# Optimization experiments

Measured on AMD Instinct MI355X. Metric: run time of the kernel, lower is better.

## Reference

```python
import jax, jax.numpy as jnp
import numpy as np

NUM_HEADS = 8
KEY_DIM = 16
D_V = 32  # attn_ratio * key_dim


def _conv1x1_bn(x, w, s, b):
    # x: [B, Cin, H, W], w: [Cout, Cin]; 1x1 conv == channel contraction,
    # eval-mode BatchNorm folded into per-channel scale s and bias b.
    y = jnp.einsum('bchw,oc->bohw', x, w)
    return y * s[:, None, None] + b[:, None, None]


def setup_inputs() -> dict:
    key = jax.random.key(0)
    ks = jax.random.split(key, 14)
    B, C, H, W = 16, 256, 32, 32
    nh_kd, dh = NUM_HEADS * KEY_DIM, NUM_HEADS * D_V
    f = jax.random.normal
    return {
        'x': f(ks[0], (B, C, H, W), jnp.float32),
        'wq': f(ks[1], (nh_kd, C), jnp.float32) * 0.05,
        'sq': jax.random.uniform(ks[2], (nh_kd,), jnp.float32),
        'bq': f(ks[3], (nh_kd,), jnp.float32) * 0.05,
        'wk': f(ks[4], (nh_kd, C), jnp.float32) * 0.05,
        'sk': jax.random.uniform(ks[5], (nh_kd,), jnp.float32),
        'bk': f(ks[6], (nh_kd,), jnp.float32) * 0.05,
        'wv': f(ks[7], (dh, C), jnp.float32) * 0.05,
        'sv': jax.random.uniform(ks[8], (dh,), jnp.float32),
        'bv': f(ks[9], (dh,), jnp.float32) * 0.05,
        'wp': f(ks[10], (C, dh), jnp.float32) * 0.05,
        'sp': jax.random.uniform(ks[11], (C,), jnp.float32),
        'bp': f(ks[12], (C,), jnp.float32) * 0.05,
    }


def reference(x, wq, sq, bq, wk, sk, bk, wv, sv, bv, wp, sp, bp):
    B, C, H, W = x.shape
    N = H * W
    # QKV projections (1x1 conv + folded BN)
    q = _conv1x1_bn(x, wq, sq, bq).reshape(B, NUM_HEADS, KEY_DIM, N)  # b h k n
    k = _conv1x1_bn(x, wk, sk, bk).reshape(B, NUM_HEADS, KEY_DIM, N)  # b h k m
    v = _conv1x1_bn(x, wv, sv, bv).reshape(B, NUM_HEADS, D_V, N)      # b h d m
    # NOTE: the original forward does NOT apply self.scale to the scores.
    attn = jnp.einsum('bhkn,bhkm->bhnm', q, k)
    attn = jax.nn.softmax(attn, axis=-1)
    out = jnp.einsum('bhnm,bhdm->bhdn', attn, v)  # b h d n
    out = out.reshape(B, NUM_HEADS * D_V, H, W)
    # proj = Sequential(activation, Conv2d_BN): activation FIRST
    out = jax.nn.relu(out)
    return _conv1x1_bn(out, wp, sp, bp)
```

## Files before the change

kernel.cpp:

```cpp
#include <hip/hip_runtime.h>

#define NTOT 1024
#define CIN  256
#define BATCH 16
#define NH   8
#define KD   16
#define DV   32
#define L2E  1.44269504088896340736f

typedef unsigned short u16;
typedef unsigned int   u32;
typedef __attribute__((ext_vector_type(8)))  _Float16 f16x8;
typedef __attribute__((ext_vector_type(16))) float    f32x16;

__device__ inline f16x8 as_f16x8(uint4 u) { return __builtin_bit_cast(f16x8, u); }
__device__ inline u32 pkrtz(float a, float b) {
  return __builtin_bit_cast(u32, __builtin_amdgcn_cvt_pkrtz(a, b));
}
__device__ inline u16 f2h(float x) {
  return __builtin_bit_cast(u16, (_Float16)x);
}
__device__ inline float fexp2(float x) {
#if __has_builtin(__builtin_amdgcn_exp2f)
  return __builtin_amdgcn_exp2f(x);
#else
  float r; asm("v_exp_f32 %0, %1" : "=v"(r) : "v"(x)); return r;
#endif
}

__global__ __launch_bounds__(64) void prep_weights(
    const float* __restrict__ wq, const float* __restrict__ sq, const float* __restrict__ bq,
    const float* __restrict__ wk, const float* __restrict__ sk, const float* __restrict__ bk,
    const float* __restrict__ wv, const float* __restrict__ sv, const float* __restrict__ bv,
    const float* __restrict__ wp, const float* __restrict__ sp, const float* __restrict__ bp,
    u16* __restrict__ wqkv, u16* __restrict__ wph, float* __restrict__ ball)
{
  const int row = blockIdx.x;
  const int t = threadIdx.x;
  const float* src; u16* dst; float sc, bi;
  if (row < 128)      { src = wq + (size_t)row*CIN;       sc = sq[row]*L2E;     bi = bq[row]*L2E;     dst = wqkv + (size_t)row*CIN; }
  else if (row < 256) { src = wk + (size_t)(row-128)*CIN; sc = sk[row-128];     bi = bk[row-128];     dst = wqkv + (size_t)row*CIN; }
  else if (row < 512) { src = wv + (size_t)(row-256)*CIN; sc = sv[row-256];     bi = bv[row-256];     dst = wqkv + (size_t)row*CIN; }
  else                { src = wp + (size_t)(row-512)*CIN; sc = sp[row-512];     bi = bp[row-512];     dst = wph + (size_t)(row-512)*CIN; }
  const float4 v = *(const float4*)&src[t*4];
  ushort4 r;
  r.x = f2h(v.x*sc); r.y = f2h(v.y*sc); r.z = f2h(v.z*sc); r.w = f2h(v.w*sc);
  *(ushort4*)&dst[t*4] = r;
  if (t == 0) ball[row] = bi;
}

__global__ __launch_bounds__(256) void transpose_x(
    const float* __restrict__ X, u16* __restrict__ Xt)
{
  __shared__ u16 T[64][64];
  const int t  = threadIdx.x;
  const int n0 = blockIdx.x * 64;
  const int c0 = blockIdx.y * 64;
  const int b  = blockIdx.z;
  #pragma unroll
  for (int rr = 0; rr < 4; ++rr) {
    const int c  = rr*16 + (t>>4);
    const int n4 = (t&15)*4;
    const float4 v = *(const float4*)&X[((size_t)b*CIN + c0 + c)*NTOT + n0 + n4];
    ushort4 r; r.x=f2h(v.x); r.y=f2h(v.y); r.z=f2h(v.z); r.w=f2h(v.w);
    *(ushort4*)&T[c][n4] = r;
  }
  __syncthreads();
  const int nl = t & 63;
  #pragma unroll
  for (int j = 0; j < 2; ++j) {
    const int oct = (t>>6)*2 + j;
    uint4 w;
    w.x = (u32)T[oct*8+0][nl] | ((u32)T[oct*8+1][nl] << 16);
    w.y = (u32)T[oct*8+2][nl] | ((u32)T[oct*8+3][nl] << 16);
    w.z = (u32)T[oct*8+4][nl] | ((u32)T[oct*8+5][nl] << 16);
    w.w = (u32)T[oct*8+6][nl] | ((u32)T[oct*8+7][nl] << 16);
    *(uint4*)&Xt[((size_t)b*NTOT + n0 + nl)*CIN + c0 + oct*8] = w;
  }
}

template<int BN, int MODE>
__global__ __launch_bounds__(256) void conv_mfma(
    const u16* __restrict__ Wh, const u16* __restrict__ Bt,
    const float* __restrict__ ball,
    u16* __restrict__ q_t, u16* __restrict__ k_t, u16* __restrict__ v_h,
    float* __restrict__ outp)
{
  constexpr int FN = BN / 64;
  __shared__ u16 A_lds[128 * 64];
  __shared__ u16 B_lds[BN * 64];
  const int t    = threadIdx.x;
  const int lane = t & 63;
  const int w    = t >> 6;
  const int wm = w >> 1, wn = w & 1;
  const int g = lane >> 5, nl = lane & 31;
  const int n0 = blockIdx.x * BN;
  const int m0 = blockIdx.y * 128;
  const int b  = blockIdx.z;

  f32x16 acc[2][FN] = {};

  for (int c0 = 0; c0 < CIN; c0 += 64) {
    #pragma unroll
    for (int r = 0; r < 4; ++r) {
      const int idx = t + r*256;
      const int row = idx >> 3, ch = idx & 7;
      const uint4 v = *(const uint4*)&Wh[(size_t)(m0+row)*CIN + c0 + ch*8];
      *(uint4*)&A_lds[row*64 + ((ch ^ (row&7))*8)] = v;
    }
    #pragma unroll
    for (int r = 0; r < BN/32; ++r) {
      const int idx = t + r*256;
      const int row = idx >> 3, ch = idx & 7;
      const uint4 v = *(const uint4*)&Bt[((size_t)b*NTOT + n0 + row)*CIN + c0 + ch*8];
      *(uint4*)&B_lds[row*64 + ((ch ^ (row&7))*8)] = v;
    }
    __syncthreads();
    #pragma unroll
    for (int ks = 0; ks < 4; ++ks) {
      const int ch = 2*ks + g;
      f16x8 a[2], bb[FN];
      #pragma unroll
      for (int fi = 0; fi < 2; ++fi) {
        const int row = wm*64 + fi*32 + nl;
        a[fi] = as_f16x8(*(const uint4*)&A_lds[row*64 + ((ch ^ (row&7))*8)]);
      }
      #pragma unroll
      for (int fj = 0; fj < FN; ++fj) {
        const int row = wn*(BN/2) + fj*32 + nl;
        bb[fj] = as_f16x8(*(const uint4*)&B_lds[row*64 + ((ch ^ (row&7))*8)]);
      }
      #pragma unroll
      for (int fi = 0; fi < 2; ++fi)
        #pragma unroll
        for (int fj = 0; fj < FN; ++fj)
          acc[fi][fj] = __builtin_amdgcn_mfma_f32_32x32x16_f16(a[fi], bb[fj], acc[fi][fj], 0, 0, 0);
    }
    __syncthreads();
  }

  #pragma unroll
  for (int fi = 0; fi < 2; ++fi) {
    #pragma unroll
    for (int fj = 0; fj < FN; ++fj) {
      const int n = n0 + wn*(BN/2) + fj*32 + nl;
      #pragma unroll
      for (int q = 0; q < 4; ++q) {
        const int ob = m0 + wm*64 + fi*32 + 8*q + 4*g;
        const float v0 = acc[fi][fj][4*q+0] + ball[ob+0];
        const float v1 = acc[fi][fj][4*q+1] + ball[ob+1];
        const float v2 = acc[fi][fj][4*q+2] + ball[ob+2];
        const float v3 = acc[fi][fj][4*q+3] + ball[ob+3];
        if (MODE == 0) {
          if (ob < 128) {
            const int h = ob >> 4, k0 = ob & 15;
            ushort4 r; r.x = f2h(v0); r.y = f2h(v1); r.z = f2h(v2); r.w = f2h(v3);
            *(ushort4*)&q_t[(((size_t)b*NH + h)*NTOT + n)*KD + k0] = r;
          } else if (ob < 256) {
            const int oo = ob - 128;
            const int h = oo >> 4, k0 = oo & 15;
            const int plane = k0 >> 3, j0 = k0 & 7;
            ushort4 r; r.x = f2h(v0); r.y = f2h(v1); r.z = f2h(v2); r.w = f2h(v3);
            *(ushort4*)&k_t[((((size_t)b*NH + h)*2 + plane)*NTOT + n)*8 + j0] = r;
          } else {
            const int oo = ob - 256;
            const int h = oo >> 5, d0 = oo & 31;
            const int mb = n >> 4, loc = n & 15;
            const int g2 = (loc >> 2) & 1;
            const int j  = (loc & 3) + ((loc >> 3) << 2);
            u16* vp = v_h + (((((size_t)b*NH + h)*64 + mb)*2 + g2)*32 + d0)*8 + j;
            vp[0*8] = f2h(v0);
            vp[1*8] = f2h(v1);
            vp[2*8] = f2h(v2);
            vp[3*8] = f2h(v3);
          }
        } else {
          float* op = outp + ((size_t)b*CIN + ob)*NTOT + n;
          op[0*NTOT] = v0; op[1*NTOT] = v1; op[2*NTOT] = v2; op[3*NTOT] = v3;
        }
      }
    }
  }
}

__global__ __launch_bounds__(1024) void attn_mfma(
    const u16* __restrict__ Qt,
    const u16* __restrict__ Kt,
    const u16* __restrict__ Vt,
    u16* __restrict__ Ot)
{
  __shared__ u16 K_lds[2*NTOT*8];
  __shared__ u16 V_lds[4096*8];
  const int t    = threadIdx.x;
  const int lane = t & 63;
  const int wave = t >> 6;
  const int bh   = blockIdx.x >> 1;
  const int half = blockIdx.x & 1;
  const int g = lane >> 5, nl = lane & 31;
  const int n0 = half*512 + wave*32;

  const u16* Kh = Kt + (size_t)bh*(2*NTOT*8);
  const u16* Vh = Vt + (size_t)bh*(4096*8);
  const u16* Qh = Qt + (size_t)bh*(NTOT*KD);

  #pragma unroll
  for (int r = 0; r < 2; ++r) {
    const int uu = r*1024 + t;
    *(uint4*)&K_lds[uu*8] = *(const uint4*)&Kh[uu*8];
  }
  #pragma unroll
  for (int r = 0; r < 4; ++r) {
    const int uu = r*1024 + t;
    *(uint4*)&V_lds[uu*8] = *(const uint4*)&Vh[uu*8];
  }

  const f16x8 qf = as_f16x8(*(const uint4*)&Qh[(size_t)(n0+nl)*KD + g*8]);
  __syncthreads();

  const f32x16 fzero = {};
  f32x16 acc = {};
  float l = 0.f;
  const char* Kb = (const char*)K_lds + g*16384 + nl*16;
  const char* Vb = (const char*)V_lds + g*512   + nl*16;

  f16x8 kf  = as_f16x8(*(const uint4*)(Kb));
  uint4 va0 = *(const uint4*)(Vb);
  uint4 va1 = *(const uint4*)(Vb + 1024);

  #pragma unroll 4
  for (int st = 0; st < 31; ++st) {
    const f32x16 s = __builtin_amdgcn_mfma_f32_32x32x16_f16(kf, qf, fzero, 0, 0, 0);
    kf  = as_f16x8(*(const uint4*)(Kb + (st+1)*512));
    const uint4 nva0 = *(const uint4*)(Vb + (st+1)*2048);
    const uint4 nva1 = *(const uint4*)(Vb + (st+1)*2048 + 1024);

    float p[16];
    #pragma unroll
    for (int r = 0; r < 16; ++r) p[r] = fexp2(s[r]);
    l += (((p[0]+p[1])+(p[2]+p[3])) + ((p[4]+p[5])+(p[6]+p[7])))
       + (((p[8]+p[9])+(p[10]+p[11])) + ((p[12]+p[13])+(p[14]+p[15])));

    uint4 b0, b1;
    b0.x = pkrtz(p[0],  p[1]);  b0.y = pkrtz(p[2],  p[3]);
    b0.z = pkrtz(p[4],  p[5]);  b0.w = pkrtz(p[6],  p[7]);
    b1.x = pkrtz(p[8],  p[9]);  b1.y = pkrtz(p[10], p[11]);
    b1.z = pkrtz(p[12], p[13]); b1.w = pkrtz(p[14], p[15]);

    acc = __builtin_amdgcn_mfma_f32_32x32x16_f16(as_f16x8(va0), as_f16x8(b0), acc, 0, 0, 0);
    acc = __builtin_amdgcn_mfma_f32_32x32x16_f16(as_f16x8(va1), as_f16x8(b1), acc, 0, 0, 0);
    va0 = nva0; va1 = nva1;
  }
  {
    const f32x16 s = __builtin_amdgcn_mfma_f32_32x32x16_f16(kf, qf, fzero, 0, 0, 0);
    float p[16];
    #pragma unroll
    for (int r = 0; r < 16; ++r) p[r] = fexp2(s[r]);
    l += (((p[0]+p[1])+(p[2]+p[3])) + ((p[4]+p[5])+(p[6]+p[7])))
       + (((p[8]+p[9])+(p[10]+p[11])) + ((p[12]+p[13])+(p[14]+p[15])));
    uint4 b0, b1;
    b0.x = pkrtz(p[0],  p[1]);  b0.y = pkrtz(p[2],  p[3]);
    b0.z = pkrtz(p[4],  p[5]);  b0.w = pkrtz(p[6],  p[7]);
    b1.x = pkrtz(p[8],  p[9]);  b1.y = pkrtz(p[10], p[11]);
    b1.z = pkrtz(p[12], p[13]); b1.w = pkrtz(p[14], p[15]);
    acc = __builtin_amdgcn_mfma_f32_32x32x16_f16(as_f16x8(va0), as_f16x8(b0), acc, 0, 0, 0);
    acc = __builtin_amdgcn_mfma_f32_32x32x16_f16(as_f16x8(va1), as_f16x8(b1), acc, 0, 0, 0);
  }

  const float lt = l + __shfl_xor(l, 32);
  const float rl = 1.0f / lt;
  const int b = bh >> 3, h = bh & 7;
  u16* op = Ot + ((size_t)b*NTOT + n0 + nl)*CIN + h*DV;
  #pragma unroll
  for (int q = 0; q < 4; ++q) {
    const float v0 = fmaxf(acc[4*q+0]*rl, 0.f);
    const float v1 = fmaxf(acc[4*q+1]*rl, 0.f);
    const float v2 = fmaxf(acc[4*q+2]*rl, 0.f);
    const float v3 = fmaxf(acc[4*q+3]*rl, 0.f);
    uint2 pk; pk.x = pkrtz(v0, v1); pk.y = pkrtz(v2, v3);
    *(uint2*)&op[8*q + 4*g] = pk;
  }
}

extern "C" void kernel_launch(void* const* d_in, const int* in_sizes, int n_in,
                              void* d_out, int out_size, void* d_ws, size_t ws_size,
                              hipStream_t stream) {
  const float* x  = (const float*)d_in[0];
  const float* wq = (const float*)d_in[1];
  const float* sq = (const float*)d_in[2];
  const float* bq = (const float*)d_in[3];
  const float* wk = (const float*)d_in[4];
  const float* sk = (const float*)d_in[5];
  const float* bk = (const float*)d_in[6];
  const float* wv = (const float*)d_in[7];
  const float* sv = (const float*)d_in[8];
  const float* bv = (const float*)d_in[9];
  const float* wp = (const float*)d_in[10];
  const float* sp = (const float*)d_in[11];
  const float* bp = (const float*)d_in[12];
  float* out = (float*)d_out;

  char* ws = (char*)d_ws;
  u16*   x_t  = (u16*)(ws);
  u16*   q_t  = (u16*)(ws + (8u  << 20));
  u16*   k_t  = (u16*)(ws + (12u << 20));
  u16*   v_h  = (u16*)(ws + (16u << 20));
  u16*   wqkv = (u16*)(ws + (24u << 20));
  u16*   wph  = (u16*)(ws + (24u << 20) + (256u << 10));
  float* ball = (float*)(ws + (24u << 20) + (384u << 10));

  prep_weights<<<dim3(768), dim3(64), 0, stream>>>(
      wq, sq, bq, wk, sk, bk, wv, sv, bv, wp, sp, bp, wqkv, wph, ball);
  transpose_x<<<dim3(16, 4, 16), dim3(256), 0, stream>>>(x, x_t);
  conv_mfma<128, 0><<<dim3(8, 4, 16), dim3(256), 0, stream>>>(
      wqkv, x_t, ball, q_t, k_t, v_h, nullptr);
  attn_mfma<<<dim3(256), dim3(1024), 0, stream>>>(q_t, k_t, v_h, x_t );
  conv_mfma<64, 1><<<dim3(16, 2, 16), dim3(256), 0, stream>>>(
      wph, x_t , ball + 512, nullptr, nullptr, nullptr, out);
}
```

Measured before the change: 68.43 us.

## Fuse prep kernels, double-buffer conv LDS, software-pipeline attention QK MFMA

```diff
diff --git a/kernel.cpp b/kernel.cpp
--- a/kernel.cpp
+++ b/kernel.cpp
@@ -10,10 +10,12 @@
 
 typedef unsigned short u16;
 typedef unsigned int   u32;
+typedef __attribute__((ext_vector_type(2)))  _Float16 f16x2;
 typedef __attribute__((ext_vector_type(8)))  _Float16 f16x8;
 typedef __attribute__((ext_vector_type(16))) float    f32x16;
 
 __device__ inline f16x8 as_f16x8(uint4 u) { return __builtin_bit_cast(f16x8, u); }
+__device__ inline f16x2 as_f16x2(u32 u)   { return __builtin_bit_cast(f16x2, u); }
 __device__ inline u32 pkrtz(float a, float b) {
   return __builtin_bit_cast(u32, __builtin_amdgcn_cvt_pkrtz(a, b));
 }
@@ -27,55 +29,64 @@
   float r; asm("v_exp_f32 %0, %1" : "=v"(r) : "v"(x)); return r;
 #endif
 }
-
-__global__ __launch_bounds__(64) void prep_weights(
+__device__ inline float dot2acc(u32 p2, float c) {
+#if __has_builtin(__builtin_amdgcn_fdot2)
+  const f16x2 one2 = __builtin_bit_cast(f16x2, (u32)0x3C003C00u);
+  return __builtin_amdgcn_fdot2(as_f16x2(p2), one2, c, false);
+#else
+  const f16x2 v = as_f16x2(p2);
+  return c + (float)v[0] + (float)v[1];
+#endif
+}
+
+__global__ __launch_bounds__(256) void prep_fused(
+    const float* __restrict__ X, u16* __restrict__ Xt,
     const float* __restrict__ wq, const float* __restrict__ sq, const float* __restrict__ bq,
     const float* __restrict__ wk, const float* __restrict__ sk, const float* __restrict__ bk,
     const float* __restrict__ wv, const float* __restrict__ sv, const float* __restrict__ bv,
     const float* __restrict__ wp, const float* __restrict__ sp, const float* __restrict__ bp,
     u16* __restrict__ wqkv, u16* __restrict__ wph, float* __restrict__ ball)
 {
-  const int row = blockIdx.x;
-  const int t = threadIdx.x;
-  const float* src; u16* dst; float sc, bi;
-  if (row < 128)      { src = wq + (size_t)row*CIN;       sc = sq[row]*L2E;     bi = bq[row]*L2E;     dst = wqkv + (size_t)row*CIN; }
-  else if (row < 256) { src = wk + (size_t)(row-128)*CIN; sc = sk[row-128];     bi = bk[row-128];     dst = wqkv + (size_t)row*CIN; }
-  else if (row < 512) { src = wv + (size_t)(row-256)*CIN; sc = sv[row-256];     bi = bv[row-256];     dst = wqkv + (size_t)row*CIN; }
-  else                { src = wp + (size_t)(row-512)*CIN; sc = sp[row-512];     bi = bp[row-512];     dst = wph + (size_t)(row-512)*CIN; }
-  const float4 v = *(const float4*)&src[t*4];
-  ushort4 r;
-  r.x = f2h(v.x*sc); r.y = f2h(v.y*sc); r.z = f2h(v.z*sc); r.w = f2h(v.w*sc);
-  *(ushort4*)&dst[t*4] = r;
-  if (t == 0) ball[row] = bi;
-}
-
-__global__ __launch_bounds__(256) void transpose_x(
-    const float* __restrict__ X, u16* __restrict__ Xt)
-{
   __shared__ u16 T[64][64];
+  const int bx = blockIdx.x;
   const int t  = threadIdx.x;
-  const int n0 = blockIdx.x * 64;
-  const int c0 = blockIdx.y * 64;
-  const int b  = blockIdx.z;
-  #pragma unroll
-  for (int rr = 0; rr < 4; ++rr) {
-    const int c  = rr*16 + (t>>4);
-    const int n4 = (t&15)*4;
-    const float4 v = *(const float4*)&X[((size_t)b*CIN + c0 + c)*NTOT + n0 + n4];
-    ushort4 r; r.x=f2h(v.x); r.y=f2h(v.y); r.z=f2h(v.z); r.w=f2h(v.w);
-    *(ushort4*)&T[c][n4] = r;
-  }
-  __syncthreads();
-  const int nl = t & 63;
-  #pragma unroll
-  for (int j = 0; j < 2; ++j) {
-    const int oct = (t>>6)*2 + j;
-    uint4 w;
-    w.x = (u32)T[oct*8+0][nl] | ((u32)T[oct*8+1][nl] << 16);
-    w.y = (u32)T[oct*8+2][nl] | ((u32)T[oct*8+3][nl] << 16);
-    w.z = (u32)T[oct*8+4][nl] | ((u32)T[oct*8+5][nl] << 16);
-    w.w = (u32)T[oct*8+6][nl] | ((u32)T[oct*8+7][nl] << 16);
-    *(uint4*)&Xt[((size_t)b*NTOT + n0 + nl)*CIN + c0 + oct*8] = w;
+  if (bx < 1024) {
+    const int n0 = (bx & 15) * 64;
+    const int c0 = ((bx >> 4) & 3) * 64;
+    const int b  = bx >> 6;
+    #pragma unroll
+    for (int rr = 0; rr < 4; ++rr) {
+      const int c  = rr*16 + (t>>4);
+      const int n4 = (t&15)*4;
+      const float4 v = *(const float4*)&X[((size_t)b*CIN + c0 + c)*NTOT + n0 + n4];
+      ushort4 r; r.x=f2h(v.x); r.y=f2h(v.y); r.z=f2h(v.z); r.w=f2h(v.w);
+      *(ushort4*)&T[c][n4] = r;
+    }
+    __syncthreads();
+    const int nl = t & 63;
+    #pragma unroll
+    for (int j = 0; j < 2; ++j) {
+      const int oct = (t>>6)*2 + j;
+      uint4 w;
+      w.x = (u32)T[oct*8+0][nl] | ((u32)T[oct*8+1][nl] << 16);
+      w.y = (u32)T[oct*8+2][nl] | ((u32)T[oct*8+3][nl] << 16);
+      w.z = (u32)T[oct*8+4][nl] | ((u32)T[oct*8+5][nl] << 16);
+      w.w = (u32)T[oct*8+6][nl] | ((u32)T[oct*8+7][nl] << 16);
+      *(uint4*)&Xt[((size_t)b*NTOT + n0 + nl)*CIN + c0 + oct*8] = w;
+    }
+  } else {
+    const int row = (bx - 1024)*4 + (t>>6);
+    const int ln  = t & 63;
+    const float* src; u16* dst; float sc, bi;
+    if (row < 128)      { src = wq + (size_t)row*CIN;       sc = sq[row]*L2E;     bi = bq[row]*L2E;     dst = wqkv + (size_t)row*CIN; }
+    else if (row < 256) { src = wk + (size_t)(row-128)*CIN; sc = sk[row-128];     bi = bk[row-128];     dst = wqkv + (size_t)row*CIN; }
+    else if (row < 512) { src = wv + (size_t)(row-256)*CIN; sc = sv[row-256];     bi = bv[row-256];     dst = wqkv + (size_t)row*CIN; }
+    else                { src = wp + (size_t)(row-512)*CIN; sc = sp[row-512];     bi = bp[row-512];     dst = wph + (size_t)(row-512)*CIN; }
+    const float4 v = *(const float4*)&src[ln*4];
+    ushort4 r;
+    r.x = f2h(v.x*sc); r.y = f2h(v.y*sc); r.z = f2h(v.z*sc); r.w = f2h(v.w*sc);
+    *(ushort4*)&dst[ln*4] = r;
+    if (ln == 0) ball[row] = bi;
   }
 }
 
@@ -87,8 +98,9 @@
     float* __restrict__ outp)
 {
   constexpr int FN = BN / 64;
-  __shared__ u16 A_lds[128 * 64];
-  __shared__ u16 B_lds[BN * 64];
+  constexpr int NB = BN / 32;
+  __shared__ u16 A_lds[2][128 * 64];
+  __shared__ u16 B_lds[2][BN * 64];
   const int t    = threadIdx.x;
   const int lane = t & 63;
   const int w    = t >> 6;
@@ -99,23 +111,45 @@
   const int b  = blockIdx.z;
 
   f32x16 acc[2][FN] = {};
-
-  for (int c0 = 0; c0 < CIN; c0 += 64) {
-    #pragma unroll
-    for (int r = 0; r < 4; ++r) {
-      const int idx = t + r*256;
-      const int row = idx >> 3, ch = idx & 7;
-      const uint4 v = *(const uint4*)&Wh[(size_t)(m0+row)*CIN + c0 + ch*8];
-      *(uint4*)&A_lds[row*64 + ((ch ^ (row&7))*8)] = v;
-    }
-    #pragma unroll
-    for (int r = 0; r < BN/32; ++r) {
-      const int idx = t + r*256;
-      const int row = idx >> 3, ch = idx & 7;
-      const uint4 v = *(const uint4*)&Bt[((size_t)b*NTOT + n0 + row)*CIN + c0 + ch*8];
-      *(uint4*)&B_lds[row*64 + ((ch ^ (row&7))*8)] = v;
-    }
-    __syncthreads();
+  uint4 rA[4], rB[NB];
+
+  #pragma unroll
+  for (int r = 0; r < 4; ++r) {
+    const int idx = t + r*256, row = idx >> 3, ch = idx & 7;
+    rA[r] = *(const uint4*)&Wh[(size_t)(m0+row)*CIN + ch*8];
+  }
+  #pragma unroll
+  for (int r = 0; r < NB; ++r) {
+    const int idx = t + r*256, row = idx >> 3, ch = idx & 7;
+    rB[r] = *(const uint4*)&Bt[((size_t)b*NTOT + n0 + row)*CIN + ch*8];
+  }
+  #pragma unroll
+  for (int r = 0; r < 4; ++r) {
+    const int idx = t + r*256, row = idx >> 3, ch = idx & 7;
+    *(uint4*)&A_lds[0][row*64 + ((ch ^ (row&7))*8)] = rA[r];
+  }
+  #pragma unroll
+  for (int r = 0; r < NB; ++r) {
+    const int idx = t + r*256, row = idx >> 3, ch = idx & 7;
+    *(uint4*)&B_lds[0][row*64 + ((ch ^ (row&7))*8)] = rB[r];
+  }
+  __syncthreads();
+
+  for (int it = 0; it < 4; ++it) {
+    const int cur = it & 1;
+    if (it < 3) {
+      const int c0 = (it+1)*64;
+      #pragma unroll
+      for (int r = 0; r < 4; ++r) {
+        const int idx = t + r*256, row = idx >> 3, ch = idx & 7;
+        rA[r] = *(const uint4*)&Wh[(size_t)(m0+row)*CIN + c0 + ch*8];
+      }
+      #pragma unroll
+      for (int r = 0; r < NB; ++r) {
+        const int idx = t + r*256, row = idx >> 3, ch = idx & 7;
+        rB[r] = *(const uint4*)&Bt[((size_t)b*NTOT + n0 + row)*CIN + c0 + ch*8];
+      }
+    }
     #pragma unroll
     for (int ks = 0; ks < 4; ++ks) {
       const int ch = 2*ks + g;
@@ -123,12 +157,12 @@
       #pragma unroll
       for (int fi = 0; fi < 2; ++fi) {
         const int row = wm*64 + fi*32 + nl;
-        a[fi] = as_f16x8(*(const uint4*)&A_lds[row*64 + ((ch ^ (row&7))*8)]);
+        a[fi] = as_f16x8(*(const uint4*)&A_lds[cur][row*64 + ((ch ^ (row&7))*8)]);
       }
       #pragma unroll
       for (int fj = 0; fj < FN; ++fj) {
         const int row = wn*(BN/2) + fj*32 + nl;
-        bb[fj] = as_f16x8(*(const uint4*)&B_lds[row*64 + ((ch ^ (row&7))*8)]);
+        bb[fj] = as_f16x8(*(const uint4*)&B_lds[cur][row*64 + ((ch ^ (row&7))*8)]);
       }
       #pragma unroll
       for (int fi = 0; fi < 2; ++fi)
@@ -136,7 +170,19 @@
         for (int fj = 0; fj < FN; ++fj)
           acc[fi][fj] = __builtin_amdgcn_mfma_f32_32x32x16_f16(a[fi], bb[fj], acc[fi][fj], 0, 0, 0);
     }
-    __syncthreads();
+    if (it < 3) {
+      #pragma unroll
+      for (int r = 0; r < 4; ++r) {
+        const int idx = t + r*256, row = idx >> 3, ch = idx & 7;
+        *(uint4*)&A_lds[cur^1][row*64 + ((ch ^ (row&7))*8)] = rA[r];
+      }
+      #pragma unroll
+      for (int r = 0; r < NB; ++r) {
+        const int idx = t + r*256, row = idx >> 3, ch = idx & 7;
+        *(uint4*)&B_lds[cur^1][row*64 + ((ch ^ (row&7))*8)] = rB[r];
+      }
+      __syncthreads();
+    }
   }
 
   #pragma unroll
@@ -226,42 +272,49 @@
   f16x8 kf  = as_f16x8(*(const uint4*)(Kb));
   uint4 va0 = *(const uint4*)(Vb);
   uint4 va1 = *(const uint4*)(Vb + 1024);
-
-  #pragma unroll 4
+  f32x16 s_cur = __builtin_amdgcn_mfma_f32_32x32x16_f16(kf, qf, fzero, 0, 0, 0);
+
+  #pragma unroll 2
   for (int st = 0; st < 31; ++st) {
-    const f32x16 s = __builtin_amdgcn_mfma_f32_32x32x16_f16(kf, qf, fzero, 0, 0, 0);
-    kf  = as_f16x8(*(const uint4*)(Kb + (st+1)*512));
+    const f16x8 kfn = as_f16x8(*(const uint4*)(Kb + (st+1)*512));
+    __builtin_amdgcn_s_setprio(1);
+    const f32x16 s_next = __builtin_amdgcn_mfma_f32_32x32x16_f16(kfn, qf, fzero, 0, 0, 0);
+    __builtin_amdgcn_s_setprio(0);
     const uint4 nva0 = *(const uint4*)(Vb + (st+1)*2048);
     const uint4 nva1 = *(const uint4*)(Vb + (st+1)*2048 + 1024);
 
     float p[16];
     #pragma unroll
-    for (int r = 0; r < 16; ++r) p[r] = fexp2(s[r]);
-    l += (((p[0]+p[1])+(p[2]+p[3])) + ((p[4]+p[5])+(p[6]+p[7])))
-       + (((p[8]+p[9])+(p[10]+p[11])) + ((p[12]+p[13])+(p[14]+p[15])));
-
+    for (int r = 0; r < 16; ++r) p[r] = fexp2(s_cur[r]);
     uint4 b0, b1;
     b0.x = pkrtz(p[0],  p[1]);  b0.y = pkrtz(p[2],  p[3]);
     b0.z = pkrtz(p[4],  p[5]);  b0.w = pkrtz(p[6],  p[7]);
     b1.x = pkrtz(p[8],  p[9]);  b1.y = pkrtz(p[10], p[11]);
     b1.z = pkrtz(p[12], p[13]); b1.w = pkrtz(p[14], p[15]);
-
+    l = dot2acc(b0.x, l); l = dot2acc(b0.y, l);
+    l = dot2acc(b0.z, l); l = dot2acc(b0.w, l);
+    l = dot2acc(b1.x, l); l = dot2acc(b1.y, l);
+    l = dot2acc(b1.z, l); l = dot2acc(b1.w, l);
+
+    __builtin_amdgcn_s_setprio(1);
     acc = __builtin_amdgcn_mfma_f32_32x32x16_f16(as_f16x8(va0), as_f16x8(b0), acc, 0, 0, 0);
     acc = __builtin_amdgcn_mfma_f32_32x32x16_f16(as_f16x8(va1), as_f16x8(b1), acc, 0, 0, 0);
-    va0 = nva0; va1 = nva1;
+    __builtin_amdgcn_s_setprio(0);
+    s_cur = s_next; va0 = nva0; va1 = nva1;
   }
   {
-    const f32x16 s = __builtin_amdgcn_mfma_f32_32x32x16_f16(kf, qf, fzero, 0, 0, 0);
     float p[16];
     #pragma unroll
-    for (int r = 0; r < 16; ++r) p[r] = fexp2(s[r]);
-    l += (((p[0]+p[1])+(p[2]+p[3])) + ((p[4]+p[5])+(p[6]+p[7])))
-       + (((p[8]+p[9])+(p[10]+p[11])) + ((p[12]+p[13])+(p[14]+p[15])));
+    for (int r = 0; r < 16; ++r) p[r] = fexp2(s_cur[r]);
     uint4 b0, b1;
     b0.x = pkrtz(p[0],  p[1]);  b0.y = pkrtz(p[2],  p[3]);
     b0.z = pkrtz(p[4],  p[5]);  b0.w = pkrtz(p[6],  p[7]);
     b1.x = pkrtz(p[8],  p[9]);  b1.y = pkrtz(p[10], p[11]);
     b1.z = pkrtz(p[12], p[13]); b1.w = pkrtz(p[14], p[15]);
+    l = dot2acc(b0.x, l); l = dot2acc(b0.y, l);
+    l = dot2acc(b0.z, l); l = dot2acc(b0.w, l);
+    l = dot2acc(b1.x, l); l = dot2acc(b1.y, l);
+    l = dot2acc(b1.z, l); l = dot2acc(b1.w, l);
     acc = __builtin_amdgcn_mfma_f32_32x32x16_f16(as_f16x8(va0), as_f16x8(b0), acc, 0, 0, 0);
     acc = __builtin_amdgcn_mfma_f32_32x32x16_f16(as_f16x8(va1), as_f16x8(b1), acc, 0, 0, 0);
   }
@@ -308,9 +361,8 @@
   u16*   wph  = (u16*)(ws + (24u << 20) + (256u << 10));
   float* ball = (float*)(ws + (24u << 20) + (384u << 10));
 
-  prep_weights<<<dim3(768), dim3(64), 0, stream>>>(
-      wq, sq, bq, wk, sk, bk, wv, sv, bv, wp, sp, bp, wqkv, wph, ball);
-  transpose_x<<<dim3(16, 4, 16), dim3(256), 0, stream>>>(x, x_t);
+  prep_fused<<<dim3(1216), dim3(256), 0, stream>>>(
+      x, x_t, wq, sq, bq, wk, sk, bk, wv, sv, bv, wp, sp, bp, wqkv, wph, ball);
   conv_mfma<128, 0><<<dim3(8, 4, 16), dim3(256), 0, stream>>>(
       wqkv, x_t, ball, q_t, k_t, v_h, nullptr);
   attn_mfma<<<dim3(256), dim3(1024), 0, stream>>>(q_t, k_t, v_h, x_t );
```

Result: faster. 57.08 us (-16.6%).
